# Performance work log

Hardware: AMD Instinct MI355X
Metric: run time of the kernel (lower is better)

## Reference

```python
import jax, jax.numpy as jnp
import numpy as np

D = 1024
H = 16
HD = 64  # head dim (bert_dim // num_heads, fixed to 64 by module)
EPS = 1e-12


def setup_inputs() -> dict:
    key = jax.random.key(0)
    ks = jax.random.split(key, 12)
    B, S1, S2 = 8, 512, 512
    scale = 0.02
    return {
        "s1_input_tensor": jax.random.normal(ks[0], (B, S1, D), jnp.float32),
        "s2_input_tensor": jax.random.normal(ks[1], (B, S2, D), jnp.float32),
        "s2_attention_mask": jnp.zeros((B, 1, 1, S2), jnp.float32),
        "Wq": jax.random.normal(ks[2], (D, D), jnp.float32) * scale,
        "bq": jnp.zeros((D,), jnp.float32),
        "Wk": jax.random.normal(ks[3], (D, D), jnp.float32) * scale,
        "bk": jnp.zeros((D,), jnp.float32),
        "Wv": jax.random.normal(ks[4], (D, D), jnp.float32) * scale,
        "bv": jnp.zeros((D,), jnp.float32),
        "Wo": jax.random.normal(ks[5], (D, D), jnp.float32) * scale,
        "bo": jnp.zeros((D,), jnp.float32),
        "ln_w": jnp.ones((D,), jnp.float32),
        "ln_b": jnp.zeros((D,), jnp.float32),
        "cl_att": 1,
    }


def _split_heads(x):
    B, S, _ = x.shape
    return x.reshape(B, S, H, HD).transpose(0, 2, 1, 3)  # [B,H,S,HD]


def _layernorm(x, w, b):
    u = jnp.mean(x, axis=-1, keepdims=True)
    s = jnp.mean(jnp.square(x - u), axis=-1, keepdims=True)
    return w * ((x - u) / jnp.sqrt(s + EPS)) + b


def reference(s1_input_tensor, s2_input_tensor, s2_attention_mask,
              Wq, bq, Wk, bk, Wv, bv, Wo, bo, ln_w, ln_b, cl_att):
    # QKV projections (dropout layers act as identity in eval)
    q = _split_heads(s1_input_tensor @ Wq + bq)   # [B,H,S1,HD]
    k = _split_heads(s2_input_tensor @ Wk + bk)   # [B,H,S2,HD]
    v = _split_heads(s2_input_tensor @ Wv + bv)   # [B,H,S2,HD]

    scores = jnp.einsum("bhqd,bhkd->bhqk", q, k) / jnp.sqrt(jnp.float32(HD))
    scores = scores + s2_attention_mask           # broadcast [B,1,1,S2]
    probs = jax.nn.softmax(scores, axis=-1)
    if cl_att:  # static Python flag: second, inverted softmax pass
        probs = jax.nn.softmax(1.0 - probs + s2_attention_mask, axis=-1)

    ctx = jnp.einsum("bhqk,bhkd->bhqd", probs, v)  # [B,H,S1,HD]
    B, _, S1, _ = ctx.shape
    ctx = ctx.transpose(0, 2, 1, 3).reshape(B, S1, D)

    # output dense + residual + LayerNorm
    h = ctx @ Wo + bo
    return _layernorm(h + s1_input_tensor, ln_w, ln_b)
```

## Files before the change

kernel.cpp:

```cpp
#include <hip/hip_runtime.h>
#include <cstdint>

#define DEV static __device__ __forceinline__

typedef __attribute__((ext_vector_type(8))) short bf16x8;
typedef __attribute__((ext_vector_type(4))) short bf16x4v;
typedef __attribute__((ext_vector_type(4))) float f32x4;

DEV float bf2f(short s) {
  union { unsigned u; float f; } c; c.u = ((unsigned)(unsigned short)s) << 16; return c.f;
}
DEV short f2bf(float f) {
  union { float f; unsigned u; } c; c.f = f;
  unsigned r = c.u + 0x7FFF + ((c.u >> 16) & 1);
  return (short)(r >> 16);
}
DEV void g2lds16(const void* g, void* l) {
  __builtin_amdgcn_global_load_lds(
      (const __attribute__((address_space(1))) void*)g,
      (__attribute__((address_space(3))) void*)l, 16, 0, 0);
}

__global__ __launch_bounds__(256) void prep_kernel(
    const float* __restrict__ s1, short* __restrict__ s1b,
    const float* __restrict__ s2, short* __restrict__ s2b,
    const float* __restrict__ w0, short* __restrict__ t0,
    const float* __restrict__ w1, short* __restrict__ t1,
    const float* __restrict__ w2, short* __restrict__ t2,
    const float* __restrict__ w3, short* __restrict__ t3) {
  __shared__ float tile[32][33];
  const int bid = blockIdx.x, tid = threadIdx.x;
  if (bid < 8192) {
    int i = bid * 256 + tid;
    const float* in = s1; short* out = s1b;
    if (i >= 1048576) { i -= 1048576; in = s2; out = s2b; }
    float4 v = reinterpret_cast<const float4*>(in)[i];
    bf16x4v o; o[0] = f2bf(v.x); o[1] = f2bf(v.y); o[2] = f2bf(v.z); o[3] = f2bf(v.w);
    reinterpret_cast<bf16x4v*>(out)[i] = o;
  } else {
    int b2 = bid - 8192;
    int z = b2 >> 10, rem = b2 & 1023;
    int bx = rem & 31, by = rem >> 5;
    int tx = tid & 31, ty = tid >> 5;
    const float* W; short* Wt;
    switch (z) {
      case 0: W = w0; Wt = t0; break;
      case 1: W = w1; Wt = t1; break;
      case 2: W = w2; Wt = t2; break;
      default: W = w3; Wt = t3; break;
    }
#pragma unroll
    for (int j = 0; j < 4; ++j)
      tile[ty + 8 * j][tx] = W[(size_t)(by * 32 + ty + 8 * j) * 1024 + bx * 32 + tx];
    __syncthreads();
#pragma unroll
    for (int j = 0; j < 4; ++j)
      Wt[(size_t)(bx * 32 + ty + 8 * j) * 1024 + by * 32 + tx] = f2bf(tile[tx][ty + 8 * j]);
  }
}

template <typename EPI>
DEV void gemm_core128(const short* __restrict__ A, const short* __restrict__ Bt,
                      int m0, int n0, EPI epi) {
  __shared__ alignas(16) short As[128 * 64];
  __shared__ alignas(16) short Bs[128 * 64];
  const int tid = threadIdx.x, lane = tid & 63, w = tid >> 6;
  const int wm = (w >> 1) * 64, wn = (w & 1) * 64;

  f32x4 acc[4][4] = {};

  for (int kt = 0; kt < 16; ++kt) {
    __syncthreads();
#pragma unroll
    for (int rnd = 0; rnd < 4; ++rnd) {
      int c = tid + rnd * 256;
      int row = c >> 3, ch = c & 7;
      g2lds16(A + (size_t)(m0 + row) * 1024 + kt * 64 + ch * 8, (char*)As + c * 16);
    }
#pragma unroll
    for (int rnd = 0; rnd < 4; ++rnd) {
      int c = tid + rnd * 256;
      int row = c >> 3, ch = c & 7;
      g2lds16(Bt + (size_t)(n0 + row) * 1024 + kt * 64 + ch * 8, (char*)Bs + c * 16);
    }
    asm volatile("s_waitcnt vmcnt(0)" ::: "memory");
    __syncthreads();
#pragma unroll
    for (int kk = 0; kk < 64; kk += 32) {
      bf16x8 a[4], b[4];
#pragma unroll
      for (int i = 0; i < 4; ++i)
        a[i] = *reinterpret_cast<const bf16x8*>(&As[(wm + i * 16 + (lane & 15)) * 64 + kk + 8 * (lane >> 4)]);
#pragma unroll
      for (int i = 0; i < 4; ++i)
        b[i] = *reinterpret_cast<const bf16x8*>(&Bs[(wn + i * 16 + (lane & 15)) * 64 + kk + 8 * (lane >> 4)]);
#pragma unroll
      for (int mi = 0; mi < 4; ++mi)
#pragma unroll
        for (int ni = 0; ni < 4; ++ni)
          acc[mi][ni] = __builtin_amdgcn_mfma_f32_16x16x32_bf16(a[mi], b[ni], acc[mi][ni], 0, 0, 0);
    }
  }
#pragma unroll
  for (int mi = 0; mi < 4; ++mi)
#pragma unroll
    for (int ni = 0; ni < 4; ++ni)
#pragma unroll
      for (int r = 0; r < 4; ++r) {
        int m = m0 + wm + mi * 16 + 4 * (lane >> 4) + r;
        int n = n0 + wn + ni * 16 + (lane & 15);
        epi(m, n, acc[mi][ni][r]);
      }
}

__global__ __launch_bounds__(256) void qkv_gemm_kernel(
    const short* __restrict__ s1b, const short* __restrict__ s2b,
    const short* __restrict__ wqt, const short* __restrict__ wkt,
    const short* __restrict__ wvt,
    const float* __restrict__ bq, const float* __restrict__ bk,
    const float* __restrict__ bv,
    short* __restrict__ qb, short* __restrict__ kb, short* __restrict__ vtb) {
  const int z = blockIdx.z;
  int flat = blockIdx.y * 8 + blockIdx.x;
  int r8 = flat & 7, q8 = flat >> 3;
  int lg = r8 * 32 + q8;
  if (z < 2) {
    const short* A = (z == 0) ? s1b : s2b;
    const short* Bt = (z == 0) ? wqt : wkt;
    const float* bias = (z == 0) ? bq : bk;
    short* out = (z == 0) ? qb : kb;
    int n0 = (lg & 7) * 128, m0 = (lg >> 3) * 128;
    gemm_core128(A, Bt, m0, n0, [&](int m, int n, float v) {
      v += bias[n];
      out[(((size_t)(m >> 9) * 16 + (n >> 6)) * 512 + (m & 511)) * 64 + (n & 63)] = f2bf(v);
    });
  } else {
    int m0 = (lg & 7) * 128, n0 = (lg >> 3) * 128;
    gemm_core128(wvt, s2b, m0, n0, [&](int m, int n, float v) {
      v += bv[m];
      vtb[(((size_t)(n >> 9) * 16 + (m >> 6)) * 64 + (m & 63)) * 512 + (n & 511)] = f2bf(v);
    });
  }
}

__global__ __launch_bounds__(256) void wo_gemm_kernel(
    const short* __restrict__ A, const short* __restrict__ Bt,
    const float* __restrict__ bias, const float* __restrict__ s1,
    float* __restrict__ out) {
  int flat = blockIdx.y * 8 + blockIdx.x;
  int r8 = flat & 7, q8 = flat >> 3;
  int lg = r8 * 32 + q8;
  int n0 = (lg & 7) * 128, m0 = (lg >> 3) * 128;
  gemm_core128(A, Bt, m0, n0, [&](int m, int n, float v) {
    out[(size_t)m * 1024 + n] = v + bias[n] + s1[(size_t)m * 1024 + n];
  });
}

__global__ __launch_bounds__(256) void attn_kernel(
    const short* __restrict__ Qg, const short* __restrict__ Kg,
    const short* __restrict__ Vtg, const float* __restrict__ maskg,
    const int* __restrict__ clp, short* __restrict__ ctx) {
  __shared__ alignas(16) short Sv[64 * 520];

  const int tid = threadIdx.x, lane = tid & 63, w = tid >> 6;
  const int l15 = lane & 15, l4 = lane >> 4;
  int flat = blockIdx.y * 8 + blockIdx.x;
  int r8 = flat & 7, q8 = flat >> 3;
  int lg = r8 * 128 + q8;
  const int qt = lg & 7, bh = lg >> 3, b = bh >> 4;
  const int cl = clp[0];
  const float* mrow = maskg + b * 512;

  const short* qbase = Qg + ((size_t)bh * 512 + qt * 64 + w * 16 + l15) * 64 + 8 * l4;
  bf16x8 qf0 = *reinterpret_cast<const bf16x8*>(qbase);
  bf16x8 qf1 = *reinterpret_cast<const bf16x8*>(qbase + 32);

  const short* kbh = Kg + (size_t)bh * 512 * 64 + 8 * l4;
  short* qrow = &Sv[(w * 16 + l15) * 520];
  for (int kt = 0; kt < 8; ++kt) {
#pragma unroll
    for (int ni = 0; ni < 4; ++ni) {
      const short* kp = kbh + (size_t)(kt * 64 + ni * 16 + l15) * 64;
      bf16x8 k0 = *reinterpret_cast<const bf16x8*>(kp);
      bf16x8 k1 = *reinterpret_cast<const bf16x8*>(kp + 32);
      f32x4 acc = {};
      __builtin_amdgcn_s_setprio(1);
      acc = __builtin_amdgcn_mfma_f32_16x16x32_bf16(k0, qf0, acc, 0, 0, 0);
      acc = __builtin_amdgcn_mfma_f32_16x16x32_bf16(k1, qf1, acc, 0, 0, 0);
      __builtin_amdgcn_s_setprio(0);
      int kb4 = kt * 64 + ni * 16 + 4 * l4;
      f32x4 mk = *reinterpret_cast<const f32x4*>(&mrow[kb4]);
      bf16x4v pk;
#pragma unroll
      for (int r = 0; r < 4; ++r) pk[r] = f2bf(acc[r] * 0.125f + mk[r]);
      *reinterpret_cast<bf16x4v*>(&qrow[kb4]) = pk;
    }
  }

  const int row = tid >> 2, sub = tid & 3;
  short* prow = &Sv[row * 520];
  float m1 = -1e30f;
#pragma unroll 4
  for (int j = 0; j < 16; ++j) {
    bf16x8 v = *reinterpret_cast<const bf16x8*>(&prow[(4 * j + sub) * 8]);
#pragma unroll
    for (int t = 0; t < 8; ++t) m1 = fmaxf(m1, bf2f(v[t]));
  }
  m1 = fmaxf(m1, __shfl_xor(m1, 1, 4));
  m1 = fmaxf(m1, __shfl_xor(m1, 2, 4));
  float Z1 = 0.f;
#pragma unroll 4
  for (int j = 0; j < 16; ++j) {
    int c0 = (4 * j + sub) * 8;
    bf16x8 v = *reinterpret_cast<const bf16x8*>(&prow[c0]);
    bf16x8 o;
#pragma unroll
    for (int t = 0; t < 8; ++t) {
      float e = __expf(bf2f(v[t]) - m1);
      Z1 += e; o[t] = f2bf(e);
    }
    *reinterpret_cast<bf16x8*>(&prow[c0]) = o;
  }
  Z1 += __shfl_xor(Z1, 1, 4); Z1 += __shfl_xor(Z1, 2, 4);
  float rZ1 = 1.0f / Z1;

  float rowscale;
  if (cl) {
    float m2 = -1e30f;
#pragma unroll 4
    for (int j = 0; j < 16; ++j) {
      int c0 = (4 * j + sub) * 8;
      bf16x8 v = *reinterpret_cast<const bf16x8*>(&prow[c0]);
      f32x4 ma = *reinterpret_cast<const f32x4*>(&mrow[c0]);
      f32x4 mb = *reinterpret_cast<const f32x4*>(&mrow[c0 + 4]);
#pragma unroll
      for (int t = 0; t < 8; ++t) {
        float msk = (t < 4) ? ma[t] : mb[t - 4];
        m2 = fmaxf(m2, 1.0f - bf2f(v[t]) * rZ1 + msk);
      }
    }
    m2 = fmaxf(m2, __shfl_xor(m2, 1, 4));
    m2 = fmaxf(m2, __shfl_xor(m2, 2, 4));
    float Z2 = 0.f;
#pragma unroll 4
    for (int j = 0; j < 16; ++j) {
      int c0 = (4 * j + sub) * 8;
      bf16x8 v = *reinterpret_cast<const bf16x8*>(&prow[c0]);
      f32x4 ma = *reinterpret_cast<const f32x4*>(&mrow[c0]);
      f32x4 mb = *reinterpret_cast<const f32x4*>(&mrow[c0 + 4]);
      bf16x8 o;
#pragma unroll
      for (int t = 0; t < 8; ++t) {
        float msk = (t < 4) ? ma[t] : mb[t - 4];
        float e = __expf(1.0f - bf2f(v[t]) * rZ1 + msk - m2);
        Z2 += e; o[t] = f2bf(e);
      }
      *reinterpret_cast<bf16x8*>(&prow[c0]) = o;
    }
    Z2 += __shfl_xor(Z2, 1, 4); Z2 += __shfl_xor(Z2, 2, 4);
    rowscale = 1.0f / Z2;
  } else {
    rowscale = rZ1;
  }

  f32x4 o[4] = {};
  const short* vbh = Vtg + (size_t)bh * 64 * 512 + 8 * l4;
  for (int kc = 0; kc < 16; ++kc) {
    bf16x8 a = *reinterpret_cast<const bf16x8*>(&Sv[(w * 16 + l15) * 520 + kc * 32 + 8 * l4]);
    bf16x8 bfr0 = *reinterpret_cast<const bf16x8*>(vbh + (size_t)(0 * 16 + l15) * 512 + kc * 32);
    bf16x8 bfr1 = *reinterpret_cast<const bf16x8*>(vbh + (size_t)(1 * 16 + l15) * 512 + kc * 32);
    bf16x8 bfr2 = *reinterpret_cast<const bf16x8*>(vbh + (size_t)(2 * 16 + l15) * 512 + kc * 32);
    bf16x8 bfr3 = *reinterpret_cast<const bf16x8*>(vbh + (size_t)(3 * 16 + l15) * 512 + kc * 32);
    __builtin_amdgcn_s_setprio(1);
    o[0] = __builtin_amdgcn_mfma_f32_16x16x32_bf16(a, bfr0, o[0], 0, 0, 0);
    o[1] = __builtin_amdgcn_mfma_f32_16x16x32_bf16(a, bfr1, o[1], 0, 0, 0);
    o[2] = __builtin_amdgcn_mfma_f32_16x16x32_bf16(a, bfr2, o[2], 0, 0, 0);
    o[3] = __builtin_amdgcn_mfma_f32_16x16x32_bf16(a, bfr3, o[3], 0, 0, 0);
    __builtin_amdgcn_s_setprio(0);
  }
  float sc[4];
#pragma unroll
  for (int r = 0; r < 4; ++r) sc[r] = __shfl(rowscale, 16 * l4 + 4 * r, 64);
  const int h = bh & 15;
#pragma unroll
  for (int ni = 0; ni < 4; ++ni)
#pragma unroll
    for (int r = 0; r < 4; ++r) {
      int s = qt * 64 + w * 16 + 4 * l4 + r;
      int d = ni * 16 + l15;
      ctx[((size_t)b * 512 + s) * 1024 + h * 64 + d] = f2bf(o[ni][r] * sc[r]);
    }
}

__global__ __launch_bounds__(256) void ln_kernel(
    const float* __restrict__ hbuf,
    const float* __restrict__ lw, const float* __restrict__ lb,
    float* __restrict__ out) {
  __shared__ float red[8];
  const int row = blockIdx.x, tid = threadIdx.x;
  float4 hv = reinterpret_cast<const float4*>(hbuf + (size_t)row * 1024)[tid];
  float x0 = hv.x, x1 = hv.y, x2 = hv.z, x3 = hv.w;
  float s = x0 + x1 + x2 + x3;
  float ss = x0 * x0 + x1 * x1 + x2 * x2 + x3 * x3;
  for (int o = 32; o; o >>= 1) { s += __shfl_down(s, o); ss += __shfl_down(ss, o); }
  int w = tid >> 6;
  if ((tid & 63) == 0) { red[w] = s; red[4 + w] = ss; }
  __syncthreads();
  float S = red[0] + red[1] + red[2] + red[3];
  float SS = red[4] + red[5] + red[6] + red[7];
  float u = S * (1.f / 1024.f);
  float var = SS * (1.f / 1024.f) - u * u;
  float inv = rsqrtf(var + 1e-12f);
  float4 wv = reinterpret_cast<const float4*>(lw)[tid];
  float4 bv = reinterpret_cast<const float4*>(lb)[tid];
  float4 ov;
  ov.x = wv.x * (x0 - u) * inv + bv.x;
  ov.y = wv.y * (x1 - u) * inv + bv.y;
  ov.z = wv.z * (x2 - u) * inv + bv.z;
  ov.w = wv.w * (x3 - u) * inv + bv.w;
  reinterpret_cast<float4*>(out + (size_t)row * 1024)[tid] = ov;
}

extern "C" void kernel_launch(void* const* d_in, const int* in_sizes, int n_in,
                              void* d_out, int out_size, void* d_ws, size_t ws_size,
                              hipStream_t stream) {
  const float* s1 = (const float*)d_in[0];
  const float* s2 = (const float*)d_in[1];
  const float* mask = (const float*)d_in[2];
  const float* Wq = (const float*)d_in[3]; const float* bq = (const float*)d_in[4];
  const float* Wk = (const float*)d_in[5]; const float* bk = (const float*)d_in[6];
  const float* Wv = (const float*)d_in[7]; const float* bv = (const float*)d_in[8];
  const float* Wo = (const float*)d_in[9]; const float* bo = (const float*)d_in[10];
  const float* lnw = (const float*)d_in[11]; const float* lnb = (const float*)d_in[12];
  const int* cl = (const int*)d_in[13];
  float* out = (float*)d_out;

  char* ws = (char*)d_ws;
  short* s1b = (short*)ws; ws += (size_t)4096 * 1024 * 2;
  short* s2b = (short*)ws; ws += (size_t)4096 * 1024 * 2;
  short* wqt = (short*)ws; ws += (size_t)1024 * 1024 * 2;
  short* wkt = (short*)ws; ws += (size_t)1024 * 1024 * 2;
  short* wvt = (short*)ws; ws += (size_t)1024 * 1024 * 2;
  short* wot = (short*)ws; ws += (size_t)1024 * 1024 * 2;
  short* qb  = (short*)ws; ws += (size_t)4096 * 1024 * 2;
  short* kb  = (short*)ws; ws += (size_t)4096 * 1024 * 2;
  short* vtb = (short*)ws; ws += (size_t)4096 * 1024 * 2;
  short* ctxb= (short*)ws; ws += (size_t)4096 * 1024 * 2;
  float* hb  = (float*)ws; ws += (size_t)4096 * 1024 * 4;

  prep_kernel<<<12288, 256, 0, stream>>>(s1, s1b, s2, s2b,
                                         Wq, wqt, Wk, wkt, Wv, wvt, Wo, wot);
  qkv_gemm_kernel<<<dim3(8, 32, 3), 256, 0, stream>>>(s1b, s2b, wqt, wkt, wvt,
                                                      bq, bk, bv, qb, kb, vtb);
  attn_kernel<<<dim3(8, 128), 256, 0, stream>>>(qb, kb, vtb, mask, cl, ctxb);
  wo_gemm_kernel<<<dim3(8, 32), 256, 0, stream>>>(ctxb, wot, bo, s1, hb);
  ln_kernel<<<4096, 256, 0, stream>>>(hb, lnw, lnb, out);
}
```

Measured before the change: 272.0 us.

## Keep attention score rows in registers instead of LDS, shuffling into MFMA A-layout

```diff
diff --git a/kernel.cpp b/kernel.cpp
--- a/kernel.cpp
+++ b/kernel.cpp
@@ -6,6 +6,7 @@
 typedef __attribute__((ext_vector_type(8))) short bf16x8;
 typedef __attribute__((ext_vector_type(4))) short bf16x4v;
 typedef __attribute__((ext_vector_type(4))) float f32x4;
+typedef __attribute__((ext_vector_type(4))) unsigned u32x4;
 
 DEV float bf2f(short s) {
   union { unsigned u; float f; } c; c.u = ((unsigned)(unsigned short)s) << 16; return c.f;
@@ -14,6 +15,11 @@
   union { float f; unsigned u; } c; c.f = f;
   unsigned r = c.u + 0x7FFF + ((c.u >> 16) & 1);
   return (short)(r >> 16);
+}
+DEV unsigned cvtpk(float lo, float hi) {
+  unsigned r;
+  asm("v_cvt_pk_bf16_f32 %0, %1, %2" : "=v"(r) : "v"(lo), "v"(hi));
+  return r;
 }
 DEV void g2lds16(const void* g, void* l) {
   __builtin_amdgcn_global_load_lds(
@@ -156,12 +162,10 @@
   });
 }
 
-__global__ __launch_bounds__(256) void attn_kernel(
+__global__ __launch_bounds__(256, 4) void attn_kernel(
     const short* __restrict__ Qg, const short* __restrict__ Kg,
     const short* __restrict__ Vtg, const float* __restrict__ maskg,
     const int* __restrict__ clp, short* __restrict__ ctx) {
-  __shared__ alignas(16) short Sv[64 * 520];
-
   const int tid = threadIdx.x, lane = tid & 63, w = tid >> 6;
   const int l15 = lane & 15, l4 = lane >> 4;
   int flat = blockIdx.y * 8 + blockIdx.x;
@@ -175,8 +179,12 @@
   bf16x8 qf0 = *reinterpret_cast<const bf16x8*>(qbase);
   bf16x8 qf1 = *reinterpret_cast<const bf16x8*>(qbase + 32);
 
+  unsigned P[64];
+  float m1 = -1e30f;
   const short* kbh = Kg + (size_t)bh * 512 * 64 + 8 * l4;
-  short* qrow = &Sv[(w * 16 + l15) * 520];
+  const bool odd = (l4 & 1);
+
+#pragma unroll
   for (int kt = 0; kt < 8; ++kt) {
 #pragma unroll
     for (int ni = 0; ni < 4; ++ni) {
@@ -184,103 +192,114 @@
       bf16x8 k0 = *reinterpret_cast<const bf16x8*>(kp);
       bf16x8 k1 = *reinterpret_cast<const bf16x8*>(kp + 32);
       f32x4 acc = {};
-      __builtin_amdgcn_s_setprio(1);
       acc = __builtin_amdgcn_mfma_f32_16x16x32_bf16(k0, qf0, acc, 0, 0, 0);
       acc = __builtin_amdgcn_mfma_f32_16x16x32_bf16(k1, qf1, acc, 0, 0, 0);
-      __builtin_amdgcn_s_setprio(0);
-      int kb4 = kt * 64 + ni * 16 + 4 * l4;
-      f32x4 mk = *reinterpret_cast<const f32x4*>(&mrow[kb4]);
-      bf16x4v pk;
-#pragma unroll
-      for (int r = 0; r < 4; ++r) pk[r] = f2bf(acc[r] * 0.125f + mk[r]);
-      *reinterpret_cast<bf16x4v*>(&qrow[kb4]) = pk;
-    }
-  }
-
-  const int row = tid >> 2, sub = tid & 3;
-  short* prow = &Sv[row * 520];
-  float m1 = -1e30f;
-#pragma unroll 4
-  for (int j = 0; j < 16; ++j) {
-    bf16x8 v = *reinterpret_cast<const bf16x8*>(&prow[(4 * j + sub) * 8]);
-#pragma unroll
-    for (int t = 0; t < 8; ++t) m1 = fmaxf(m1, bf2f(v[t]));
-  }
-  m1 = fmaxf(m1, __shfl_xor(m1, 1, 4));
-  m1 = fmaxf(m1, __shfl_xor(m1, 2, 4));
+      f32x4 mk = *reinterpret_cast<const f32x4*>(&mrow[kt * 64 + ni * 16 + 4 * l4]);
+      float s0 = fmaf(acc[0], 0.125f, mk[0]);
+      float s1v = fmaf(acc[1], 0.125f, mk[1]);
+      float s2v = fmaf(acc[2], 0.125f, mk[2]);
+      float s3 = fmaf(acc[3], 0.125f, mk[3]);
+      m1 = fmaxf(m1, fmaxf(fmaxf(s0, s1v), fmaxf(s2v, s3)));
+      unsigned pk0 = cvtpk(s0, s1v), pk1 = cvtpk(s2v, s3);
+      unsigned e0 = __shfl_xor(pk0, 16), e1 = __shfl_xor(pk1, 16);
+      unsigned h0 = odd ? e0 : pk0;
+      unsigned h1 = odd ? e1 : pk1;
+      unsigned h2 = odd ? pk0 : e0;
+      unsigned h3 = odd ? pk1 : e1;
+      unsigned g0 = __shfl_xor(h0, 32), g1 = __shfl_xor(h1, 32);
+      unsigned g2 = __shfl_xor(h2, 32), g3 = __shfl_xor(h3, 32);
+      bool ist = (((l4 >> 1) & 1) == (ni & 1));
+      bool useh = ((l4 & 1) == (ni & 1));
+      unsigned w0 = useh ? h0 : g0;
+      unsigned w1 = useh ? h1 : g1;
+      unsigned w2 = useh ? h2 : g2;
+      unsigned w3 = useh ? h3 : g3;
+      const int mIdx = kt * 2 + (ni >> 1);
+      P[4 * mIdx + 0] = ist ? w0 : P[4 * mIdx + 0];
+      P[4 * mIdx + 1] = ist ? w1 : P[4 * mIdx + 1];
+      P[4 * mIdx + 2] = ist ? w2 : P[4 * mIdx + 2];
+      P[4 * mIdx + 3] = ist ? w3 : P[4 * mIdx + 3];
+    }
+  }
+
+  m1 = fmaxf(m1, __shfl_xor(m1, 16));
+  m1 = fmaxf(m1, __shfl_xor(m1, 32));
   float Z1 = 0.f;
-#pragma unroll 4
-  for (int j = 0; j < 16; ++j) {
-    int c0 = (4 * j + sub) * 8;
-    bf16x8 v = *reinterpret_cast<const bf16x8*>(&prow[c0]);
-    bf16x8 o;
-#pragma unroll
-    for (int t = 0; t < 8; ++t) {
-      float e = __expf(bf2f(v[t]) - m1);
-      Z1 += e; o[t] = f2bf(e);
-    }
-    *reinterpret_cast<bf16x8*>(&prow[c0]) = o;
-  }
-  Z1 += __shfl_xor(Z1, 1, 4); Z1 += __shfl_xor(Z1, 2, 4);
+#pragma unroll
+  for (int i = 0; i < 64; ++i) {
+    unsigned u = P[i];
+    float lo = __uint_as_float(u << 16);
+    float hi = __uint_as_float(u & 0xffff0000u);
+    float e0 = __expf(lo - m1), e1 = __expf(hi - m1);
+    Z1 += e0 + e1;
+    P[i] = cvtpk(e0, e1);
+  }
+  Z1 += __shfl_xor(Z1, 16); Z1 += __shfl_xor(Z1, 32);
   float rZ1 = 1.0f / Z1;
-
-  float rowscale;
+  float rowscale = rZ1;
+
   if (cl) {
     float m2 = -1e30f;
-#pragma unroll 4
-    for (int j = 0; j < 16; ++j) {
-      int c0 = (4 * j + sub) * 8;
-      bf16x8 v = *reinterpret_cast<const bf16x8*>(&prow[c0]);
-      f32x4 ma = *reinterpret_cast<const f32x4*>(&mrow[c0]);
-      f32x4 mb = *reinterpret_cast<const f32x4*>(&mrow[c0 + 4]);
-#pragma unroll
-      for (int t = 0; t < 8; ++t) {
-        float msk = (t < 4) ? ma[t] : mb[t - 4];
-        m2 = fmaxf(m2, 1.0f - bf2f(v[t]) * rZ1 + msk);
+#pragma unroll
+    for (int m = 0; m < 16; ++m) {
+      f32x4 mka = *reinterpret_cast<const f32x4*>(&mrow[32 * m + 8 * l4]);
+      f32x4 mkb = *reinterpret_cast<const f32x4*>(&mrow[32 * m + 8 * l4 + 4]);
+#pragma unroll
+      for (int j = 0; j < 4; ++j) {
+        unsigned u = P[4 * m + j];
+        float p0 = __uint_as_float(u << 16) * rZ1;
+        float p1 = __uint_as_float(u & 0xffff0000u) * rZ1;
+        float mv0 = (j < 2) ? mka[2 * j] : mkb[2 * j - 4];
+        float mv1 = (j < 2) ? mka[2 * j + 1] : mkb[2 * j - 3];
+        m2 = fmaxf(m2, fmaxf(1.0f - p0 + mv0, 1.0f - p1 + mv1));
       }
     }
-    m2 = fmaxf(m2, __shfl_xor(m2, 1, 4));
-    m2 = fmaxf(m2, __shfl_xor(m2, 2, 4));
+    m2 = fmaxf(m2, __shfl_xor(m2, 16));
+    m2 = fmaxf(m2, __shfl_xor(m2, 32));
     float Z2 = 0.f;
-#pragma unroll 4
-    for (int j = 0; j < 16; ++j) {
-      int c0 = (4 * j + sub) * 8;
-      bf16x8 v = *reinterpret_cast<const bf16x8*>(&prow[c0]);
-      f32x4 ma = *reinterpret_cast<const f32x4*>(&mrow[c0]);
-      f32x4 mb = *reinterpret_cast<const f32x4*>(&mrow[c0 + 4]);
-      bf16x8 o;
-#pragma unroll
-      for (int t = 0; t < 8; ++t) {
-        float msk = (t < 4) ? ma[t] : mb[t - 4];
-        float e = __expf(1.0f - bf2f(v[t]) * rZ1 + msk - m2);
-        Z2 += e; o[t] = f2bf(e);
+#pragma unroll
+    for (int m = 0; m < 16; ++m) {
+      f32x4 mka = *reinterpret_cast<const f32x4*>(&mrow[32 * m + 8 * l4]);
+      f32x4 mkb = *reinterpret_cast<const f32x4*>(&mrow[32 * m + 8 * l4 + 4]);
+#pragma unroll
+      for (int j = 0; j < 4; ++j) {
+        unsigned u = P[4 * m + j];
+        float p0 = __uint_as_float(u << 16) * rZ1;
+        float p1 = __uint_as_float(u & 0xffff0000u) * rZ1;
+        float mv0 = (j < 2) ? mka[2 * j] : mkb[2 * j - 4];
+        float mv1 = (j < 2) ? mka[2 * j + 1] : mkb[2 * j - 3];
+        float e0 = __expf(1.0f - p0 + mv0 - m2);
+        float e1 = __expf(1.0f - p1 + mv1 - m2);
+        Z2 += e0 + e1;
+        P[4 * m + j] = cvtpk(e0, e1);
       }
-      *reinterpret_cast<bf16x8*>(&prow[c0]) = o;
-    }
-    Z2 += __shfl_xor(Z2, 1, 4); Z2 += __shfl_xor(Z2, 2, 4);
+    }
+    Z2 += __shfl_xor(Z2, 16); Z2 += __shfl_xor(Z2, 32);
     rowscale = 1.0f / Z2;
-  } else {
-    rowscale = rZ1;
   }
 
   f32x4 o[4] = {};
   const short* vbh = Vtg + (size_t)bh * 64 * 512 + 8 * l4;
-  for (int kc = 0; kc < 16; ++kc) {
-    bf16x8 a = *reinterpret_cast<const bf16x8*>(&Sv[(w * 16 + l15) * 520 + kc * 32 + 8 * l4]);
-    bf16x8 bfr0 = *reinterpret_cast<const bf16x8*>(vbh + (size_t)(0 * 16 + l15) * 512 + kc * 32);
-    bf16x8 bfr1 = *reinterpret_cast<const bf16x8*>(vbh + (size_t)(1 * 16 + l15) * 512 + kc * 32);
-    bf16x8 bfr2 = *reinterpret_cast<const bf16x8*>(vbh + (size_t)(2 * 16 + l15) * 512 + kc * 32);
-    bf16x8 bfr3 = *reinterpret_cast<const bf16x8*>(vbh + (size_t)(3 * 16 + l15) * 512 + kc * 32);
+#pragma unroll
+  for (int m = 0; m < 16; ++m) {
+    u32x4 av;
+    av[0] = P[4 * m + 0]; av[1] = P[4 * m + 1];
+    av[2] = P[4 * m + 2]; av[3] = P[4 * m + 3];
+    bf16x8 a = __builtin_bit_cast(bf16x8, av);
+    bf16x8 b0 = *reinterpret_cast<const bf16x8*>(vbh + (size_t)(0 * 16 + l15) * 512 + m * 32);
+    bf16x8 b1 = *reinterpret_cast<const bf16x8*>(vbh + (size_t)(1 * 16 + l15) * 512 + m * 32);
+    bf16x8 b2 = *reinterpret_cast<const bf16x8*>(vbh + (size_t)(2 * 16 + l15) * 512 + m * 32);
+    bf16x8 b3 = *reinterpret_cast<const bf16x8*>(vbh + (size_t)(3 * 16 + l15) * 512 + m * 32);
     __builtin_amdgcn_s_setprio(1);
-    o[0] = __builtin_amdgcn_mfma_f32_16x16x32_bf16(a, bfr0, o[0], 0, 0, 0);
-    o[1] = __builtin_amdgcn_mfma_f32_16x16x32_bf16(a, bfr1, o[1], 0, 0, 0);
-    o[2] = __builtin_amdgcn_mfma_f32_16x16x32_bf16(a, bfr2, o[2], 0, 0, 0);
-    o[3] = __builtin_amdgcn_mfma_f32_16x16x32_bf16(a, bfr3, o[3], 0, 0, 0);
+    o[0] = __builtin_amdgcn_mfma_f32_16x16x32_bf16(a, b0, o[0], 0, 0, 0);
+    o[1] = __builtin_amdgcn_mfma_f32_16x16x32_bf16(a, b1, o[1], 0, 0, 0);
+    o[2] = __builtin_amdgcn_mfma_f32_16x16x32_bf16(a, b2, o[2], 0, 0, 0);
+    o[3] = __builtin_amdgcn_mfma_f32_16x16x32_bf16(a, b3, o[3], 0, 0, 0);
     __builtin_amdgcn_s_setprio(0);
   }
   float sc[4];
 #pragma unroll
-  for (int r = 0; r < 4; ++r) sc[r] = __shfl(rowscale, 16 * l4 + 4 * r, 64);
+  for (int r = 0; r < 4; ++r) sc[r] = __shfl(rowscale, 4 * l4 + r);
   const int h = bh & 15;
 #pragma unroll
   for (int ni = 0; ni < 4; ++ni)
```

Result: slower. 282.2 us (+3.7%).
